# Kernel tuning notes

Measured on AMD Instinct MI355X. Metric: run time of the kernel, lower is better.

## Reference

```python
import jax, jax.numpy as jnp
import numpy as np
from jax import lax

L, B, S, D, V, NL = 64, 32, 64, 512, 32000, 2


def setup_inputs() -> dict:
    key = jax.random.key(0)
    ks = jax.random.split(key, 9)
    sd = 1.0 / np.sqrt(D)
    return {
        "rnn_input": jax.random.randint(ks[0], (L, B), 0, V),
        "last_hidden": jax.random.normal(ks[1], (NL, B, D), jnp.float32),
        "encoder_outputs": jax.random.normal(ks[2], (S, B, D), jnp.float32),
        "embed_table": jax.random.normal(ks[3], (V, D), jnp.float32) * sd,
        "sru_W": jax.random.normal(ks[4], (NL, D, 3 * D), jnp.float32) * sd,
        "sru_b": jax.random.normal(ks[5], (NL, 2 * D), jnp.float32) * 0.01,
        "attn_W": jax.random.normal(ks[6], (2 * D, D), jnp.float32) * sd,
        "out_W": jax.random.normal(ks[7], (D, V), jnp.float32) * sd,
        "out_b": jax.random.normal(ks[8], (V,), jnp.float32) * 0.01,
    }


def _sru_layer(x, c0, W, b):
    # x: [L,B,D] layer input, c0: [B,D], W: [D,3D], b: [2D]
    U = jnp.einsum('lbd,de->lbe', x, W)          # [L,B,3D]
    z, fp, rp = jnp.split(U, 3, axis=-1)          # candidate, forget, reset pre-acts
    bf, br = jnp.split(b, 2)
    f = jax.nn.sigmoid(fp + bf)
    r = jax.nn.sigmoid(rp + br)

    def step(c, inp):
        f_t, z_t = inp
        c = f_t * c + (1.0 - f_t) * z_t
        return c, c

    c_last, c_seq = lax.scan(step, c0, (f, z))    # c_seq: [L,B,D]
    h = r * jnp.tanh(c_seq) + (1.0 - r) * x       # highway (n_in == n_out)
    return h, c_last


def reference(rnn_input, last_hidden, encoder_outputs, embed_table, sru_W, sru_b, attn_W, out_W, out_b):
    x = embed_table[rnn_input]                    # [L,B,D]
    finals = []
    for l in range(NL):                           # small fixed layer loop
        x, c_last = _sru_layer(x, last_hidden[l], sru_W[l], sru_b[l])
        finals.append(c_last)
    hidden = jnp.stack(finals, axis=0)            # [NL,B,D]

    q = jnp.transpose(x, (1, 0, 2))               # [B,L,D]
    mem = jnp.transpose(encoder_outputs, (1, 0, 2))  # [B,S,D]
    scores = jnp.einsum('bld,bsd->bls', q, mem)   # dot attention
    align = jax.nn.softmax(scores, axis=-1)
    ctx = jnp.einsum('bls,bsd->bld', align, mem)
    attn_h = jnp.tanh(jnp.concatenate([ctx, q], axis=-1) @ attn_W)  # [B,L,D]
    output = attn_h @ out_W + out_b               # [B,L,V]
    return output, hidden
```

## Files before the change

kernel.cpp:

```cpp
#include <hip/hip_runtime.h>
#include <hip/hip_bf16.h>

#define L_ 64
#define B_ 32
#define S_ 64
#define D_ 512
#define V_ 32000
#define NL_ 2

typedef __attribute__((ext_vector_type(8))) short bf16x8;
typedef __attribute__((ext_vector_type(4))) float f32x4;

static __device__ __forceinline__ short f2bf(float f) {
  union { float f; unsigned u; } x; x.f = f;
  unsigned r = (x.u + 0x7FFFu + ((x.u >> 16) & 1u)) >> 16;
  return (short)r;
}

#define GLOAD_LDS16(g, l)                                                     \
  __builtin_amdgcn_global_load_lds(                                           \
      (const __attribute__((address_space(1))) void*)(g),                     \
      (__attribute__((address_space(3))) void*)(l), 16, 0, 0)

__global__ void prep_kernel(const float* __restrict__ sruW, const float* __restrict__ attnW,
                            const float* __restrict__ outW, const int* __restrict__ tok,
                            const float* __restrict__ tab,
                            short* __restrict__ WTs, short* __restrict__ WTa,
                            short* __restrict__ WTo,
                            float* __restrict__ xf, short* __restrict__ xb) {
  int bid = blockIdx.x;
  int tx = threadIdx.x, ty = threadIdx.y;
  __shared__ float tile[32][33];
  if (bid < 18048) {
    const float* in;
    short* out;
    int K, N, bx, by;
    if (bid < 1536) {
      int l = bid >> 9 >= 1 ? (bid >= 768) : 0;
      l = (bid >= 768) ? 1 : 0;
      int r = bid - l * 768;
      bx = r % 48; by = r / 48; K = 512; N = 1536;
      in = sruW + (size_t)l * 512 * 1536;
      out = WTs + (size_t)l * 1536 * 512;
    } else if (bid < 2048) {
      int r = bid - 1536;
      bx = r % 16; by = r / 16; K = 1024; N = 512;
      in = attnW; out = WTa;
    } else {
      int r = bid - 2048;
      bx = r % 1000; by = r / 1000; K = 512; N = 32000;
      in = outW; out = WTo;
    }
    int x = bx * 32 + tx;
    int y0 = by * 32;
    for (int j = ty; j < 32; j += 8) {
      int y = y0 + j;
      tile[j][tx] = (x < N && y < K) ? in[(size_t)y * N + x] : 0.f;
    }
    __syncthreads();
    int xo = y0 + tx;
    int yo0 = bx * 32;
    for (int j = ty; j < 32; j += 8) {
      int yo = yo0 + j;
      if (yo < N && xo < K) out[(size_t)yo * K + xo] = f2bf(tile[tx][j]);
    }
  } else {
    int i = (bid - 18048) * 256 + ty * 32 + tx;
    int d = i & (D_ - 1);
    int lb = i >> 9;
    float v = tab[(size_t)tok[lb] * D_ + d];
    xf[i] = v;
    xb[i] = f2bf(v);
  }
}

template <int BMt, int BNt, int WM, int WN, int MODE>
__global__ __launch_bounds__(256) void gemm_t(
    const short* __restrict__ A, const short* __restrict__ BT,
    void* __restrict__ Cptr, const float* __restrict__ bias,
    int M, int N, int K, int nbm) {
  constexpr int MI = BMt / WM / 16;
  constexpr int NI = BNt / WN / 16;
  constexpr int ACH = BMt / 8;
  constexpr int NCH = (BMt + BNt) / 8;
  constexpr int CPW = NCH / 4;

  const int nwg = gridDim.x;
  const int qc = nwg >> 3;
  const int bid = blockIdx.x;
  const int wg = (bid & 7) * qc + (bid >> 3);
  const int bm = wg % nbm;
  const int bn = wg / nbm;

  __shared__ __align__(16) short la[2][BMt * 64];
  __shared__ __align__(16) short lb[2][BNt * 64];
  const int tid = threadIdx.x;
  const int wave = tid >> 6, lane = tid & 63;
  const int wm = (wave / WN) * (BMt / WM);
  const int wn = (wave % WN) * (BNt / WN);

  f32x4 acc[MI][NI] = {};

  const int lrow = lane >> 3;
  const int lslot = lane & 7;
  const short* Abase = A + (size_t)(bm * BMt) * K;
  const short* Bbase = BT + (size_t)(bn * BNt) * K;

  auto stage = [&](int buf, int k0) {
#pragma unroll
    for (int c = 0; c < CPW; ++c) {
      int chunk = wave * CPW + c;
      if (chunk < ACH) {
        int row = chunk * 8 + lrow;
        int slot = lslot ^ (row & 7);
        GLOAD_LDS16(Abase + (size_t)row * K + k0 + slot * 8, &la[buf][chunk * 512]);
      } else {
        int bc = chunk - ACH;
        int row = bc * 8 + lrow;
        int slot = lslot ^ (row & 7);
        GLOAD_LDS16(Bbase + (size_t)row * K + k0 + slot * 8, &lb[buf][bc * 512]);
      }
    }
  };

  stage(0, 0);
  __syncthreads();

  const int nt = K / 64;
  int cur = 0;
  for (int t = 0; t < nt; ++t) {
    if (t + 1 < nt) stage(cur ^ 1, (t + 1) * 64);
#pragma unroll
    for (int kk = 0; kk < 2; ++kk) {
      bf16x8 af[MI], bfr[NI];
#pragma unroll
      for (int mi = 0; mi < MI; ++mi) {
        int row = wm + mi * 16 + (lane & 15);
        int slot = (kk * 4 + (lane >> 4)) ^ (row & 7);
        af[mi] = *(const bf16x8*)&la[cur][row * 64 + slot * 8];
      }
#pragma unroll
      for (int ni = 0; ni < NI; ++ni) {
        int row = wn + ni * 16 + (lane & 15);
        int slot = (kk * 4 + (lane >> 4)) ^ (row & 7);
        bfr[ni] = *(const bf16x8*)&lb[cur][row * 64 + slot * 8];
      }
#pragma unroll
      for (int mi = 0; mi < MI; ++mi)
#pragma unroll
        for (int ni = 0; ni < NI; ++ni)
          acc[mi][ni] = __builtin_amdgcn_mfma_f32_16x16x32_bf16(
              af[mi], bfr[ni], acc[mi][ni], 0, 0, 0);
    }
    __syncthreads();
    cur ^= 1;
  }

  const int cl = lane & 15;
  const int rl = (lane >> 4) * 4;
#pragma unroll
  for (int mi = 0; mi < MI; ++mi) {
#pragma unroll
    for (int ni = 0; ni < NI; ++ni) {
      int c = bn * BNt + wn + ni * 16 + cl;
      int r0 = bm * BMt + wm + mi * 16 + rl;
      float bs = (MODE == 2) ? bias[c] : 0.f;
#pragma unroll
      for (int j = 0; j < 4; ++j) {
        int r = r0 + j;
        float v = acc[mi][ni][j];
        if (MODE == 0) {
          ((float*)Cptr)[(size_t)r * N + c] = v;
        } else if (MODE == 1) {
          ((short*)Cptr)[(size_t)r * N + c] = f2bf(tanhf(v));
        } else {
          int b = r & 31, l = r >> 5;
          ((float*)Cptr)[(size_t)(b * L_ + l) * N + c] = v + bs;
        }
      }
    }
  }
}

__global__ void sru_scan_kernel(const float* __restrict__ U, const float* __restrict__ bvec,
                                const float* __restrict__ xin, const float* __restrict__ c0,
                                float* __restrict__ hf, short* __restrict__ hb,
                                float* __restrict__ clast) {
  int idx = blockIdx.x * 64 + threadIdx.x;
  int b = idx >> 9, d = idx & 511;
  float c = c0[idx];
  const float bfb = bvec[d], brb = bvec[512 + d];
  const float* Ub = U + (size_t)b * 1536 + d;
  const float* Xb = xin + (size_t)b * 512 + d;

  for (int l0 = 0; l0 < L_; l0 += 8) {
    float z[8], fp[8], rp[8], xv[8];
#pragma unroll
    for (int j = 0; j < 8; ++j) {
      size_t u = (size_t)(l0 + j) * B_ * 1536;
      z[j] = Ub[u];
      fp[j] = Ub[u + 512];
      rp[j] = Ub[u + 1024];
      xv[j] = Xb[(size_t)(l0 + j) * B_ * 512];
    }
#pragma unroll
    for (int j = 0; j < 8; ++j) {
      float f = 1.f / (1.f + expf(-(fp[j] + bfb)));
      float r = 1.f / (1.f + expf(-(rp[j] + brb)));
      c = f * c + (1.f - f) * z[j];
      float h = r * tanhf(c) + (1.f - r) * xv[j];
      size_t o = ((size_t)(l0 + j) * B_ + b) * 512 + d;
      hf[o] = h;
      hb[o] = f2bf(h);
    }
  }
  clast[idx] = c;
}

__global__ __launch_bounds__(256) void attn_fused_kernel(
    const float* __restrict__ x, const float* __restrict__ enc,
    const short* __restrict__ xq, short* __restrict__ cat) {
  __shared__ float q[512];
  __shared__ float al[64];
  int r = blockIdx.x;
  int b = r & (B_ - 1);
  int tid = threadIdx.x;
  int wave = tid >> 6, lane = tid & 63;
  for (int d = tid; d < 512; d += 256) {
    q[d] = x[(size_t)r * 512 + d];
    cat[(size_t)r * 1024 + 512 + d] = xq[(size_t)r * 512 + d];
  }
  __syncthreads();
#pragma unroll
  for (int si = 0; si < 16; ++si) {
    int s = wave * 16 + si;
    const float* m = enc + ((size_t)s * B_ + b) * 512;
    float a = 0.f;
#pragma unroll
    for (int k = 0; k < 8; ++k) a += q[lane + k * 64] * m[lane + k * 64];
    for (int o = 32; o > 0; o >>= 1) a += __shfl_xor(a, o);
    if (lane == 0) al[s] = a;
  }
  __syncthreads();
  if (tid < 64) {
    float v = al[tid];
    float mx = v;
    for (int o = 32; o > 0; o >>= 1) mx = fmaxf(mx, __shfl_xor(mx, o));
    float e = expf(v - mx);
    float sm = e;
    for (int o = 32; o > 0; o >>= 1) sm += __shfl_xor(sm, o);
    al[tid] = e / sm;
  }
  __syncthreads();
  for (int d = tid; d < 512; d += 256) {
    float acc = 0.f;
#pragma unroll 16
    for (int s = 0; s < S_; ++s) acc += al[s] * enc[((size_t)s * B_ + b) * 512 + d];
    cat[(size_t)r * 1024 + d] = f2bf(acc);
  }
}

extern "C" void kernel_launch(void* const* d_in, const int* in_sizes, int n_in,
                              void* d_out, int out_size, void* d_ws, size_t ws_size,
                              hipStream_t stream) {
  const int* rnn = (const int*)d_in[0];
  const float* h0 = (const float*)d_in[1];
  const float* enc = (const float*)d_in[2];
  const float* tab = (const float*)d_in[3];
  const float* sruW = (const float*)d_in[4];
  const float* srub = (const float*)d_in[5];
  const float* attnW = (const float*)d_in[6];
  const float* outW = (const float*)d_in[7];
  const float* outb = (const float*)d_in[8];
  float* out = (float*)d_out;

  char* ws = (char*)d_ws;
  size_t off = 0;
  auto alloc = [&](size_t bytes) {
    char* p = ws + off;
    off += (bytes + 255) & ~(size_t)255;
    return p;
  };
  float* xf = (float*)alloc(4ull * 2048 * 512);
  float* xf2 = (float*)alloc(4ull * 2048 * 512);
  short* xb = (short*)alloc(2ull * 2048 * 512);
  float* U = (float*)alloc(4ull * 2048 * 1536);
  short* WTs = (short*)alloc(2ull * 2 * 1536 * 512);
  short* WTa = (short*)alloc(2ull * 512 * 1024);
  short* WTo = (short*)alloc(2ull * 32000 * 512);
  short* cat = (short*)alloc(2ull * 2048 * 1024);
  short* ah = (short*)alloc(2ull * 2048 * 512);

  prep_kernel<<<22144, dim3(32, 8), 0, stream>>>(sruW, attnW, outW, rnn, tab,
                                                 WTs, WTa, WTo, xf, xb);

  float* hidden_out = out + (size_t)B_ * L_ * V_;

  gemm_t<64, 128, 1, 4, 0><<<384, 256, 0, stream>>>(xb, WTs, U, nullptr, 2048, 1536, 512, 32);
  sru_scan_kernel<<<256, 64, 0, stream>>>(U, srub, xf, h0, xf2, xb, hidden_out);
  gemm_t<64, 128, 1, 4, 0><<<384, 256, 0, stream>>>(xb, WTs + 1536 * 512, U, nullptr,
                                                    2048, 1536, 512, 32);
  sru_scan_kernel<<<256, 64, 0, stream>>>(U, srub + 1024, xf2, h0 + B_ * D_, xf, xb,
                                          hidden_out + B_ * D_);

  attn_fused_kernel<<<2048, 256, 0, stream>>>(xf, enc, xb, cat);

  gemm_t<64, 64, 2, 2, 1><<<256, 256, 0, stream>>>(cat, WTa, ah, nullptr, 2048, 512, 1024, 32);
  gemm_t<128, 128, 2, 2, 2><<<4000, 256, 0, stream>>>(ah, WTo, out, outb, 2048, 32000, 512, 16);
}
```

Before: 244.7 us.

## Replace output projection GEMM with 256x256-tile 8-wave pipelined kernel

Adds a new GEMM kernel for the large output projection (2048x32000x512). It uses 256x256 tiles, 512 threads, swizzled LDS double buffering via direct global-to-LDS loads, interleaved staging with MFMA, and XCD-aware block remapping. The aim is to raise data reuse per tile and overlap loads with compute in the dominant GEMM. The larger tile gives only 1000 workgroups and one block per CU, so occupancy and tail balance are the risk. The change also includes small cleanups in the prep and old epilogue code.

```diff
diff --git a/kernel.cpp b/kernel.cpp
--- a/kernel.cpp
+++ b/kernel.cpp
@@ -36,8 +36,7 @@
     short* out;
     int K, N, bx, by;
     if (bid < 1536) {
-      int l = bid >> 9 >= 1 ? (bid >= 768) : 0;
-      l = (bid >= 768) ? 1 : 0;
+      int l = (bid >= 768) ? 1 : 0;
       int r = bid - l * 768;
       bx = r % 48; by = r / 48; K = 512; N = 1536;
       in = sruW + (size_t)l * 512 * 1536;
@@ -164,7 +163,6 @@
     for (int ni = 0; ni < NI; ++ni) {
       int c = bn * BNt + wn + ni * 16 + cl;
       int r0 = bm * BMt + wm + mi * 16 + rl;
-      float bs = (MODE == 2) ? bias[c] : 0.f;
 #pragma unroll
       for (int j = 0; j < 4; ++j) {
         int r = r0 + j;
@@ -175,7 +173,160 @@
           ((short*)Cptr)[(size_t)r * N + c] = f2bf(tanhf(v));
         } else {
           int b = r & 31, l = r >> 5;
+          ((float*)Cptr)[(size_t)(b * L_ + l) * N + c] = v + bias[c];
+        }
+      }
+    }
+  }
+}
+
+template <int MODE>
+__global__ __launch_bounds__(512, 1) void gemm8p_kernel(
+    const short* __restrict__ A, const short* __restrict__ BT,
+    void* __restrict__ Cptr, const float* __restrict__ bias,
+    int M, int N, int K, int nbm) {
+  const int nwg = gridDim.x;
+  const int qc = nwg >> 3;
+  const int bid = blockIdx.x;
+  const int wg = (bid & 7) * qc + (bid >> 3);
+  const int bm = wg % nbm;
+  const int bn = wg / nbm;
+
+  __shared__ __align__(16) short la[4 * 8192];
+  __shared__ __align__(16) short lb[4 * 8192];
+
+  const int tid = threadIdx.x;
+  const int wave = tid >> 6, lane = tid & 63;
+  const int wr = wave >> 2;
+  const int wc = wave & 3;
+  const int fr = lane & 15;
+
+  f32x4 acc[8][4] = {};
+
+  const short* Abase = A + (size_t)(bm * 256) * K;
+  const short* Bbase = BT + (size_t)(bn * 256) * K;
+  const int nt = K / 64;
+
+  const int s_row = tid >> 3;
+  const int s_slot = tid & 7;
+  auto stageA = [&](int W, int kt, int mh) {
+#pragma unroll
+    for (int i = 0; i < 2; ++i) {
+      int rih = i * 64 + s_row;
+      int grow = ((rih >> 6) << 7) + (mh << 6) + (rih & 63);
+      int k = kt * 64 + ((s_slot ^ (rih & 7)) << 3);
+      GLOAD_LDS16(Abase + (size_t)grow * K + k,
+                  &la[(W * 2 + mh) * 8192 + (i * 512 + tid) * 8]);
+    }
+  };
+  auto stageB = [&](int W, int kt, int hb) {
+#pragma unroll
+    for (int i = 0; i < 2; ++i) {
+      int rih = i * 64 + s_row;
+      int grow = ((rih >> 6) << 7) + (hb << 6) + (rih & 63);
+      int k = kt * 64 + ((s_slot ^ (rih & 7)) << 3);
+      GLOAD_LDS16(Bbase + (size_t)grow * K + k,
+                  &lb[(W * 2 + hb) * 8192 + (i * 512 + tid) * 8]);
+    }
+  };
+
+  int arow[4], brow[4], aslot[2];
+#pragma unroll
+  for (int q = 0; q < 4; ++q) {
+    arow[q] = (wr * 64 + q * 16 + fr) * 64;
+    brow[q] = ((wc >> 1) * 64 + q * 16 + fr) * 64 + (wc & 1) * 8192;
+  }
+#pragma unroll
+  for (int kk = 0; kk < 2; ++kk) aslot[kk] = ((kk * 4 + (lane >> 4)) ^ (lane & 7)) * 8;
+
+  stageB(0, 0, 0);
+  stageB(0, 0, 1);
+  stageA(0, 0, 0);
+  stageA(0, 0, 1);
+  asm volatile("s_waitcnt vmcnt(2)\n\ts_barrier" ::: "memory");
+
+  for (int kt = 0; kt < nt; ++kt) {
+    const int R = kt & 1, W = R ^ 1;
+    const int baseA = R * 16384;
+    const int baseB = R * 16384;
+    const bool more = (kt + 1 < nt);
+    bf16x8 b0[4], b1[4], a[4];
+
+    if (more) stageB(W, kt + 1, 0);
+#pragma unroll
+    for (int ni = 0; ni < 4; ++ni) b0[ni] = *(const bf16x8*)&lb[baseB + brow[ni] + aslot[0]];
+#pragma unroll
+    for (int q = 0; q < 4; ++q) a[q] = *(const bf16x8*)&la[baseA + arow[q] + aslot[0]];
+    __builtin_amdgcn_s_setprio(1);
+#pragma unroll
+    for (int q = 0; q < 4; ++q)
+#pragma unroll
+      for (int ni = 0; ni < 4; ++ni)
+        acc[q][ni] = __builtin_amdgcn_mfma_f32_16x16x32_bf16(a[q], b0[ni], acc[q][ni], 0, 0, 0);
+    __builtin_amdgcn_s_setprio(0);
+
+    if (more) stageB(W, kt + 1, 1);
+#pragma unroll
+    for (int ni = 0; ni < 4; ++ni) b1[ni] = *(const bf16x8*)&lb[baseB + brow[ni] + aslot[1]];
+#pragma unroll
+    for (int q = 0; q < 4; ++q) a[q] = *(const bf16x8*)&la[baseA + arow[q] + aslot[1]];
+    __builtin_amdgcn_s_setprio(1);
+#pragma unroll
+    for (int q = 0; q < 4; ++q)
+#pragma unroll
+      for (int ni = 0; ni < 4; ++ni)
+        acc[q][ni] = __builtin_amdgcn_mfma_f32_16x16x32_bf16(a[q], b1[ni], acc[q][ni], 0, 0, 0);
+    __builtin_amdgcn_s_setprio(0);
+
+    if (more) {
+      asm volatile("s_waitcnt vmcnt(4)\n\ts_barrier" ::: "memory");
+    } else {
+      asm volatile("s_waitcnt vmcnt(0)\n\ts_barrier" ::: "memory");
+    }
+
+    if (more) stageA(W, kt + 1, 0);
+#pragma unroll
+    for (int q = 0; q < 4; ++q) a[q] = *(const bf16x8*)&la[baseA + 8192 + arow[q] + aslot[0]];
+    __builtin_amdgcn_s_setprio(1);
+#pragma unroll
+    for (int q = 0; q < 4; ++q)
+#pragma unroll
+      for (int ni = 0; ni < 4; ++ni)
+        acc[4 + q][ni] = __builtin_amdgcn_mfma_f32_16x16x32_bf16(a[q], b0[ni], acc[4 + q][ni], 0, 0, 0);
+    __builtin_amdgcn_s_setprio(0);
+
+    if (more) stageA(W, kt + 1, 1);
+#pragma unroll
+    for (int q = 0; q < 4; ++q) a[q] = *(const bf16x8*)&la[baseA + 8192 + arow[q] + aslot[1]];
+    __builtin_amdgcn_s_setprio(1);
+#pragma unroll
+    for (int q = 0; q < 4; ++q)
+#pragma unroll
+      for (int ni = 0; ni < 4; ++ni)
+        acc[4 + q][ni] = __builtin_amdgcn_mfma_f32_16x16x32_bf16(a[q], b1[ni], acc[4 + q][ni], 0, 0, 0);
+    __builtin_amdgcn_s_setprio(0);
+
+    if (more) {
+      asm volatile("s_waitcnt lgkmcnt(0) vmcnt(2)\n\ts_barrier" ::: "memory");
+    }
+  }
+
+#pragma unroll
+  for (int mi = 0; mi < 8; ++mi) {
+#pragma unroll
+    for (int ni = 0; ni < 4; ++ni) {
+      int c = bn * 256 + wc * 64 + ni * 16 + fr;
+      int r0 = bm * 256 + wr * 128 + mi * 16 + (lane >> 4) * 4;
+      float bs = (MODE == 2) ? bias[c] : 0.f;
+#pragma unroll
+      for (int j = 0; j < 4; ++j) {
+        int r = r0 + j;
+        float v = acc[mi][ni][j];
+        if (MODE == 2) {
+          int b = r & 31, l = r >> 5;
           ((float*)Cptr)[(size_t)(b * L_ + l) * N + c] = v + bs;
+        } else {
+          ((float*)Cptr)[(size_t)r * N + c] = v;
         }
       }
     }
@@ -306,5 +457,5 @@
   attn_fused_kernel<<<2048, 256, 0, stream>>>(xf, enc, xb, cat);
 
   gemm_t<64, 64, 2, 2, 1><<<256, 256, 0, stream>>>(cat, WTa, ah, nullptr, 2048, 512, 1024, 32);
-  gemm_t<128, 128, 2, 2, 2><<<4000, 256, 0, stream>>>(ah, WTo, out, outb, 2048, 32000, 512, 16);
-}
+  gemm8p_kernel<2><<<1000, 512, 0, stream>>>(ah, WTo, out, outb, 2048, 32000, 512, 8);
+}
```

After: 254.7 us. 1.04x slower.

## Add single-buffered swizzled 128x128 GEMM with XCD-aware block remap for output projection

Applied to the files above, without the earlier changes.

Introduces a new gemm_s kernel for the vocabulary projection. It single-buffers LDS with an XOR-swizzled layout and uses launch_bounds for 3 blocks per CU. Block IDs are remapped so that consecutive blocks spread across the 8 XCDs, and neighbouring M tiles sharing a B tile land on the same XCD to improve L2 reuse. Dropping double buffering may expose load latency, which the higher occupancy is meant to hide.

```diff
diff --git a/kernel.cpp b/kernel.cpp
--- a/kernel.cpp
+++ b/kernel.cpp
@@ -36,8 +36,7 @@
     short* out;
     int K, N, bx, by;
     if (bid < 1536) {
-      int l = bid >> 9 >= 1 ? (bid >= 768) : 0;
-      l = (bid >= 768) ? 1 : 0;
+      int l = (bid >= 768) ? 1 : 0;
       int r = bid - l * 768;
       bx = r % 48; by = r / 48; K = 512; N = 1536;
       in = sruW + (size_t)l * 512 * 1536;
@@ -164,7 +163,6 @@
     for (int ni = 0; ni < NI; ++ni) {
       int c = bn * BNt + wn + ni * 16 + cl;
       int r0 = bm * BMt + wm + mi * 16 + rl;
-      float bs = (MODE == 2) ? bias[c] : 0.f;
 #pragma unroll
       for (int j = 0; j < 4; ++j) {
         int r = r0 + j;
@@ -175,7 +173,93 @@
           ((short*)Cptr)[(size_t)r * N + c] = f2bf(tanhf(v));
         } else {
           int b = r & 31, l = r >> 5;
+          ((float*)Cptr)[(size_t)(b * L_ + l) * N + c] = v + bias[c];
+        }
+      }
+    }
+  }
+}
+
+template <int MODE>
+__global__ __launch_bounds__(256, 3) void gemm_s(
+    const short* __restrict__ A, const short* __restrict__ BT,
+    void* __restrict__ Cptr, const float* __restrict__ bias,
+    int M, int N, int K, int nbm) {
+  const int nwg = gridDim.x;
+  const int qc = nwg >> 3;
+  const int bid = blockIdx.x;
+  const int wg = (bid & 7) * qc + (bid >> 3);
+  const int bm = wg % nbm;
+  const int bn = wg / nbm;
+
+  __shared__ __align__(16) short la[128 * 64];
+  __shared__ __align__(16) short lb[128 * 64];
+  const int tid = threadIdx.x;
+  const int wave = tid >> 6, lane = tid & 63;
+  const int wm = (wave >> 1) * 64, wn = (wave & 1) * 64;
+
+  f32x4 acc[4][4] = {};
+
+  const int lrow = lane >> 3;
+  const int lslot = lane & 7;
+  const short* Abase = A + (size_t)(bm * 128) * K;
+  const short* Bbase = BT + (size_t)(bn * 128) * K;
+
+  const int nt = K / 64;
+  for (int t = 0; t < nt; ++t) {
+    const int k0 = t * 64;
+#pragma unroll
+    for (int c = 0; c < 4; ++c) {
+      int chunk = wave * 4 + c;
+      int row = chunk * 8 + lrow;
+      int slot = lslot ^ (row & 7);
+      GLOAD_LDS16(Abase + (size_t)row * K + k0 + slot * 8, &la[chunk * 512]);
+      GLOAD_LDS16(Bbase + (size_t)row * K + k0 + slot * 8, &lb[chunk * 512]);
+    }
+    __syncthreads();
+#pragma unroll
+    for (int kk = 0; kk < 2; ++kk) {
+      bf16x8 af[4], bfr[4];
+#pragma unroll
+      for (int mi = 0; mi < 4; ++mi) {
+        int row = wm + mi * 16 + (lane & 15);
+        int slot = (kk * 4 + (lane >> 4)) ^ (row & 7);
+        af[mi] = *(const bf16x8*)&la[row * 64 + slot * 8];
+      }
+#pragma unroll
+      for (int ni = 0; ni < 4; ++ni) {
+        int row = wn + ni * 16 + (lane & 15);
+        int slot = (kk * 4 + (lane >> 4)) ^ (row & 7);
+        bfr[ni] = *(const bf16x8*)&lb[row * 64 + slot * 8];
+      }
+#pragma unroll
+      for (int mi = 0; mi < 4; ++mi)
+#pragma unroll
+        for (int ni = 0; ni < 4; ++ni)
+          acc[mi][ni] = __builtin_amdgcn_mfma_f32_16x16x32_bf16(
+              af[mi], bfr[ni], acc[mi][ni], 0, 0, 0);
+    }
+    __syncthreads();
+  }
+
+  const int cl = lane & 15;
+  const int rl = (lane >> 4) * 4;
+#pragma unroll
+  for (int mi = 0; mi < 4; ++mi) {
+#pragma unroll
+    for (int ni = 0; ni < 4; ++ni) {
+      int c = bn * 128 + wn + ni * 16 + cl;
+      int r0 = bm * 128 + wm + mi * 16 + rl;
+      float bs = (MODE == 2) ? bias[c] : 0.f;
+#pragma unroll
+      for (int j = 0; j < 4; ++j) {
+        int r = r0 + j;
+        float v = acc[mi][ni][j];
+        if (MODE == 2) {
+          int b = r & 31, l = r >> 5;
           ((float*)Cptr)[(size_t)(b * L_ + l) * N + c] = v + bs;
+        } else {
+          ((float*)Cptr)[(size_t)r * N + c] = v;
         }
       }
     }
@@ -306,5 +390,5 @@
   attn_fused_kernel<<<2048, 256, 0, stream>>>(xf, enc, xb, cat);
 
   gemm_t<64, 64, 2, 2, 1><<<256, 256, 0, stream>>>(cat, WTa, ah, nullptr, 2048, 512, 1024, 32);
-  gemm_t<128, 128, 2, 2, 2><<<4000, 256, 0, stream>>>(ah, WTo, out, outb, 2048, 32000, 512, 16);
-}
+  gemm_s<2><<<4000, 256, 0, stream>>>(ah, WTo, out, outb, 2048, 32000, 512, 16);
+}
```

After: 231.7 us. 1.06x faster.
